# Optimization experiments

Hardware: AMD Instinct MI355X
Metric: run time of the kernel (lower is better)

The kernel has to match this reference:

```python
import jax, jax.numpy as jnp
import numpy as np

DT_RANK = 64
D_STATE = 16


def setup_inputs() -> dict:
    key = jax.random.key(0)
    ks = jax.random.split(key, 6)
    B, L, Di = 2, 2048, 2048
    x = jax.random.normal(ks[0], (B, L, Di), dtype=jnp.float32)
    W_xproj = jax.random.normal(ks[1], (DT_RANK + 2 * D_STATE, Di), dtype=jnp.float32) * (Di ** -0.5)
    W_dt = jax.random.uniform(ks[2], (Di, DT_RANK), dtype=jnp.float32, minval=-(DT_RANK ** -0.5), maxval=DT_RANK ** -0.5)
    dt = jnp.exp(jax.random.uniform(ks[3], (Di,), dtype=jnp.float32) * (np.log(0.1) - np.log(0.001)) + np.log(0.001))
    b_dt = dt + jnp.log(-jnp.expm1(-dt))
    A_log = jnp.log(jnp.broadcast_to(jnp.arange(1, D_STATE + 1, dtype=jnp.float32), (Di, D_STATE)))
    D_param = jnp.ones((Di,), dtype=jnp.float32)
    return {"x": x, "W_xproj": W_xproj, "W_dt": W_dt, "b_dt": b_dt, "A_log": A_log, "D_param": D_param}


def _selective_scan(u, delta, A, Bm, Cm):
    # u, delta: (b, l, d); A: (d, n); Bm, Cm: (b, l, n)
    deltaA = jnp.exp(delta[..., None] * A[None, None])          # (b, l, d, n)
    deltaB_u = delta[..., None] * Bm[:, :, None, :] * u[..., None]  # (b, l, d, n)

    def step(h, inp):
        dA, dBu, c = inp                      # dA,dBu: (b,d,n); c: (b,n)
        h = dA * h + dBu
        y = jnp.einsum('bdn,bn->bd', h, c)
        return h, y

    b, l, d = u.shape
    h0 = jnp.zeros((b, d, A.shape[1]), dtype=u.dtype)
    xs = (jnp.moveaxis(deltaA, 1, 0), jnp.moveaxis(deltaB_u, 1, 0), jnp.moveaxis(Cm, 1, 0))
    _, ys = jax.lax.scan(step, h0, xs)        # ys: (l, b, d)
    return jnp.moveaxis(ys, 0, 1)


def reference(x, W_xproj, W_dt, b_dt, A_log, D_param):
    x_dbl = jnp.einsum('bld,ed->ble', x, W_xproj)  # (b, l, dt_rank + 2*n)
    dlt = x_dbl[..., :DT_RANK]
    Bm = x_dbl[..., DT_RANK:DT_RANK + D_STATE]
    Cm = x_dbl[..., DT_RANK + D_STATE:]
    delta = jax.nn.softplus(jnp.einsum('blr,dr->bld', dlt, W_dt) + b_dt)
    A = -jnp.exp(A_log.astype(jnp.float32))
    y = _selective_scan(x, delta, A, Bm, Cm)
    return y + x * D_param[None, None, :]
```

## Files before the change

### kernel.cpp

```cpp
#include <hip/hip_runtime.h>

#define BATCH 2
#define L_SEQ 2048
#define DI 2048
#define NROW (BATCH * L_SEQ)
#define E_DIM 96
#define RNK 64
#define NST 16
#define NCH 64
#define CL 32
#define SPLITK 16
#define KSL (DI / SPLITK)

#define WS_XDBL 0
#define WS_PART 393216
#define WS_HLOC 393216
#define WS_DSUM (393216 + 4194304)

__device__ __forceinline__ float softplusf(float z) {
    return fmaxf(z, 0.f) + __logf(1.f + __expf(-fabsf(z)));
}

__global__ __launch_bounds__(256) void gemm_xproj_part(const float* __restrict__ x,
                                                       const float* __restrict__ Wx,
                                                       float* __restrict__ part) {
    __shared__ float xs[32][68];
    __shared__ float wsh[32][100];
    const int tid = threadIdx.x;
    const int r0 = blockIdx.x * 64;
    const int kbase0 = blockIdx.y * KSL;
    const int rg = tid >> 4;
    const int cg = tid & 15;

    float acc[4][6];
#pragma unroll
    for (int i = 0; i < 4; i++)
#pragma unroll
        for (int j = 0; j < 6; j++) acc[i][j] = 0.f;

    for (int kt = 0; kt < KSL / 32; kt++) {
        const int kb = kbase0 + kt * 32;
#pragma unroll
        for (int rep = 0; rep < 2; rep++) {
            int i = rep * 256 + tid;
            int row = i >> 3;
            int kq = i & 7;
            float4 v = *(const float4*)&x[(long)(r0 + row) * DI + kb + kq * 4];
            xs[kq * 4 + 0][row] = v.x;
            xs[kq * 4 + 1][row] = v.y;
            xs[kq * 4 + 2][row] = v.z;
            xs[kq * 4 + 3][row] = v.w;
        }
#pragma unroll
        for (int rep = 0; rep < 3; rep++) {
            int i = rep * 256 + tid;
            int e = i >> 3;
            int kq = i & 7;
            float4 v = *(const float4*)&Wx[(long)e * DI + kb + kq * 4];
            wsh[kq * 4 + 0][e] = v.x;
            wsh[kq * 4 + 1][e] = v.y;
            wsh[kq * 4 + 2][e] = v.z;
            wsh[kq * 4 + 3][e] = v.w;
        }
        __syncthreads();
#pragma unroll 8
        for (int k = 0; k < 32; k++) {
            float xr[4], wr[6];
#pragma unroll
            for (int i = 0; i < 4; i++) xr[i] = xs[k][rg * 4 + i];
#pragma unroll
            for (int j = 0; j < 6; j++) wr[j] = wsh[k][cg * 6 + j];
#pragma unroll
            for (int i = 0; i < 4; i++)
#pragma unroll
                for (int j = 0; j < 6; j++) acc[i][j] = fmaf(xr[i], wr[j], acc[i][j]);
        }
        __syncthreads();
    }
    const long sbase = (long)blockIdx.y * NROW * E_DIM;
#pragma unroll
    for (int i = 0; i < 4; i++) {
        long rowb = sbase + (long)(r0 + rg * 4 + i) * E_DIM + cg * 6;
#pragma unroll
        for (int j = 0; j < 6; j++) part[rowb + j] = acc[i][j];
    }
}

__global__ __launch_bounds__(256) void xproj_reduce(const float* __restrict__ part,
                                                    float* __restrict__ xdbl) {
    const int i4 = blockIdx.x * 256 + threadIdx.x;
    const float4* p4 = (const float4*)part;
    float4 s = p4[i4];
#pragma unroll
    for (int sp = 1; sp < SPLITK; sp++) {
        float4 v = p4[(long)sp * (NROW * E_DIM / 4) + i4];
        s.x += v.x; s.y += v.y; s.z += v.z; s.w += v.w;
    }
    ((float4*)xdbl)[i4] = s;
}

__global__ __launch_bounds__(256) void scan_carry_fused(const float* __restrict__ x,
                                                        const float* __restrict__ xdbl,
                                                        const float* __restrict__ Wdt,
                                                        const float* __restrict__ bdt,
                                                        const float* __restrict__ A_log,
                                                        float* __restrict__ delta_out,
                                                        float* __restrict__ hloc,
                                                        float* __restrict__ dsumb) {
    const int tid = threadIdx.x;
    const int d = blockIdx.x * 256 + tid;
    const int c = blockIdx.y;
    const int b = blockIdx.z;
    const int row0 = b * L_SEQ + c * CL;

    float wdtr[64];
#pragma unroll
    for (int q = 0; q < 16; q++) {
        float4 v = *(const float4*)&Wdt[(long)d * RNK + q * 4];
        wdtr[q * 4 + 0] = v.x; wdtr[q * 4 + 1] = v.y;
        wdtr[q * 4 + 2] = v.z; wdtr[q * 4 + 3] = v.w;
    }
    const float bd = bdt[d];

    float A[16];
#pragma unroll
    for (int q = 0; q < 4; q++) {
        float4 v = *(const float4*)&A_log[(long)d * NST + q * 4];
        A[q * 4 + 0] = -__expf(v.x);
        A[q * 4 + 1] = -__expf(v.y);
        A[q * 4 + 2] = -__expf(v.z);
        A[q * 4 + 3] = -__expf(v.w);
    }
    float h[16];
#pragma unroll
    for (int n = 0; n < 16; n++) h[n] = 0.f;
    float dsum = 0.f;

    long idx = (long)row0 * DI + d;
    float xn = x[idx];
    const float* __restrict__ rp = xdbl + (long)row0 * E_DIM;
    for (int ll = 0; ll < CL; ll++) {
        float xc = xn;
        if (ll + 1 < CL) xn = x[idx + DI];
        float dv0 = 0.f, dv1 = 0.f, dv2 = 0.f, dv3 = 0.f;
#pragma unroll
        for (int q = 0; q < 16; q++) {
            dv0 = fmaf(rp[q * 4 + 0], wdtr[q * 4 + 0], dv0);
            dv1 = fmaf(rp[q * 4 + 1], wdtr[q * 4 + 1], dv1);
            dv2 = fmaf(rp[q * 4 + 2], wdtr[q * 4 + 2], dv2);
            dv3 = fmaf(rp[q * 4 + 3], wdtr[q * 4 + 3], dv3);
        }
        float dc = softplusf(((dv0 + dv1) + (dv2 + dv3)) + bd);
        delta_out[idx] = dc;
        float du = dc * xc;
#pragma unroll
        for (int n = 0; n < 16; n++)
            h[n] = fmaf(__expf(dc * A[n]), h[n], du * rp[64 + n]);
        dsum += dc;
        idx += DI;
        rp += E_DIM;
    }

    const long cb = ((long)(b * NCH + c) * DI + d);
#pragma unroll
    for (int q = 0; q < 4; q++)
        *(float4*)&hloc[cb * 16 + q * 4] =
            make_float4(h[q * 4], h[q * 4 + 1], h[q * 4 + 2], h[q * 4 + 3]);
    dsumb[cb] = dsum;
}

__global__ __launch_bounds__(256) void scan_prefix(const float* __restrict__ A_log,
                                                   float* __restrict__ hloc,
                                                   const float* __restrict__ dsumb) {
    const int g = blockIdx.x * 256 + threadIdx.x;
    const int n = g & 15;
    const int d = (g >> 4) & (DI - 1);
    const int b = g >> 15;
    const float An = -__expf(A_log[(long)d * NST + n]);
    float hc = 0.f;
    for (int c = 0; c < NCH; c++) {
        const long cb = ((long)(b * NCH + c) * DI + d);
        float hl = hloc[cb * 16 + n];
        float dsv = dsumb[cb];
        hloc[cb * 16 + n] = hc;
        hc = fmaf(__expf(An * dsv), hc, hl);
    }
}

__global__ __launch_bounds__(256) void scan_out(const float* __restrict__ x,
                                                const float* __restrict__ xdbl,
                                                const float* __restrict__ A_log,
                                                const float* __restrict__ Dp,
                                                const float* __restrict__ hloc,
                                                float* __restrict__ out) {
    const int tid = threadIdx.x;
    const int d = blockIdx.x * 256 + tid;
    const int c = blockIdx.y;
    const int b = blockIdx.z;
    const int row0 = b * L_SEQ + c * CL;

    float A[16];
#pragma unroll
    for (int q = 0; q < 4; q++) {
        float4 v = *(const float4*)&A_log[(long)d * NST + q * 4];
        A[q * 4 + 0] = -__expf(v.x);
        A[q * 4 + 1] = -__expf(v.y);
        A[q * 4 + 2] = -__expf(v.z);
        A[q * 4 + 3] = -__expf(v.w);
    }
    float h[16];
    const long cb = ((long)(b * NCH + c) * DI + d);
#pragma unroll
    for (int q = 0; q < 4; q++) {
        float4 v = *(const float4*)&hloc[cb * 16 + q * 4];
        h[q * 4 + 0] = v.x; h[q * 4 + 1] = v.y; h[q * 4 + 2] = v.z; h[q * 4 + 3] = v.w;
    }
    const float Dd = Dp[d];

    long idx = (long)row0 * DI + d;
    float dn = out[idx], xn = x[idx];
    const float* __restrict__ rp = xdbl + (long)row0 * E_DIM;
    for (int ll = 0; ll < CL; ll++) {
        float dc = dn, xc = xn;
        long nidx = (ll + 1 < CL) ? idx + DI : idx;
        dn = out[nidx];
        xn = x[nidx];
        float du = dc * xc;
        float y = 0.f;
#pragma unroll
        for (int n = 0; n < 16; n++) {
            h[n] = fmaf(__expf(dc * A[n]), h[n], du * rp[64 + n]);
            y = fmaf(h[n], rp[80 + n], y);
        }
        out[idx] = fmaf(xc, Dd, y);
        idx += DI;
        rp += E_DIM;
    }
}

extern "C" void kernel_launch(void* const* d_in, const int* in_sizes, int n_in,
                              void* d_out, int out_size, void* d_ws, size_t ws_size,
                              hipStream_t stream) {
    const float* x    = (const float*)d_in[0];
    const float* Wx   = (const float*)d_in[1];
    const float* Wdt  = (const float*)d_in[2];
    const float* bdt  = (const float*)d_in[3];
    const float* Alog = (const float*)d_in[4];
    const float* Dp   = (const float*)d_in[5];
    float* out = (float*)d_out;
    float* ws = (float*)d_ws;
    float* xdbl  = ws + WS_XDBL;
    float* partb = ws + WS_PART;
    float* hloc  = ws + WS_HLOC;
    float* dsumb = ws + WS_DSUM;

    gemm_xproj_part<<<dim3(NROW / 64, SPLITK), 256, 0, stream>>>(x, Wx, partb);
    xproj_reduce<<<dim3(NROW * E_DIM / 4 / 256), 256, 0, stream>>>(partb, xdbl);
    scan_carry_fused<<<dim3(DI / 256, NCH, BATCH), 256, 0, stream>>>(x, xdbl, Wdt, bdt,
                                                                     Alog, out, hloc, dsumb);
    scan_prefix<<<dim3(BATCH * DI * NST / 256), 256, 0, stream>>>(Alog, hloc, dsumb);
    scan_out<<<dim3(DI / 256, NCH, BATCH), 256, 0, stream>>>(x, xdbl, Alog, Dp, hloc, out);
}
```

Baseline: 216.4 us.

## Split delta projection into tiled shared-memory GEMM and stage B/C in LDS

Moves the dt-rank projection and softplus out of the scan carry kernel into a dedicated register- and LDS-tiled GEMM that writes delta to the output buffer. The scan kernels read delta from memory and load each chunk's B and C rows into shared memory once per block, rather than every thread reading them from global memory. This removes the 64-float Wdt register array and the per-thread 64-FMA dot product from the latency-bound scan. The cost is an extra kernel launch plus a full write and re-read of delta through global memory.

New measurement: 201.5 us. 6.9% less time.

```diff
diff --git a/kernel.cpp b/kernel.cpp
--- a/kernel.cpp
+++ b/kernel.cpp
@@ -99,28 +99,95 @@
     ((float4*)xdbl)[i4] = s;
 }
 
-__global__ __launch_bounds__(256) void scan_carry_fused(const float* __restrict__ x,
-                                                        const float* __restrict__ xdbl,
-                                                        const float* __restrict__ Wdt,
-                                                        const float* __restrict__ bdt,
-                                                        const float* __restrict__ A_log,
-                                                        float* __restrict__ delta_out,
-                                                        float* __restrict__ hloc,
-                                                        float* __restrict__ dsumb) {
+__global__ __launch_bounds__(256) void gemm_dt(const float* __restrict__ xdbl,
+                                               const float* __restrict__ Wdt,
+                                               const float* __restrict__ b_dt,
+                                               float* __restrict__ delta) {
+    __shared__ float dl[32][68];
+    __shared__ float wt[32][132];
+    const int tid = threadIdx.x;
+    const int row0 = blockIdx.x * 64;
+    const int d0 = blockIdx.y * 128;
+    const int rg = tid >> 5;
+    const int cg = tid & 31;
+
+    float acc[8][4];
+#pragma unroll
+    for (int i = 0; i < 8; i++)
+#pragma unroll
+        for (int j = 0; j < 4; j++) acc[i][j] = 0.f;
+
+    for (int kt = 0; kt < 2; kt++) {
+        const int kb = kt * 32;
+#pragma unroll
+        for (int rep = 0; rep < 2; rep++) {
+            int i = rep * 256 + tid;
+            int row = i >> 3;
+            int kq = i & 7;
+            float4 v = *(const float4*)&xdbl[(long)(row0 + row) * E_DIM + kb + kq * 4];
+            dl[kq * 4 + 0][row] = v.x;
+            dl[kq * 4 + 1][row] = v.y;
+            dl[kq * 4 + 2][row] = v.z;
+            dl[kq * 4 + 3][row] = v.w;
+        }
+#pragma unroll
+        for (int rep = 0; rep < 4; rep++) {
+            int i = rep * 256 + tid;
+            int col = i >> 3;
+            int kq = i & 7;
+            float4 v = *(const float4*)&Wdt[(long)(d0 + col) * RNK + kb + kq * 4];
+            wt[kq * 4 + 0][col] = v.x;
+            wt[kq * 4 + 1][col] = v.y;
+            wt[kq * 4 + 2][col] = v.z;
+            wt[kq * 4 + 3][col] = v.w;
+        }
+        __syncthreads();
+#pragma unroll 8
+        for (int k = 0; k < 32; k++) {
+            float xr[8], wr[4];
+#pragma unroll
+            for (int i = 0; i < 8; i++) xr[i] = dl[k][rg * 8 + i];
+#pragma unroll
+            for (int j = 0; j < 4; j++) wr[j] = wt[k][cg * 4 + j];
+#pragma unroll
+            for (int i = 0; i < 8; i++)
+#pragma unroll
+                for (int j = 0; j < 4; j++) acc[i][j] = fmaf(xr[i], wr[j], acc[i][j]);
+        }
+        __syncthreads();
+    }
+
+    float4 bb = *(const float4*)&b_dt[d0 + cg * 4];
+#pragma unroll
+    for (int i = 0; i < 8; i++) {
+        int row = row0 + rg * 8 + i;
+        float4 o;
+        o.x = softplusf(acc[i][0] + bb.x);
+        o.y = softplusf(acc[i][1] + bb.y);
+        o.z = softplusf(acc[i][2] + bb.z);
+        o.w = softplusf(acc[i][3] + bb.w);
+        *(float4*)&delta[(long)row * DI + d0 + cg * 4] = o;
+    }
+}
+
+__global__ __launch_bounds__(256) void scan_carry(const float* __restrict__ x,
+                                                  const float* __restrict__ delta,
+                                                  const float* __restrict__ xdbl,
+                                                  const float* __restrict__ A_log,
+                                                  float* __restrict__ hloc,
+                                                  float* __restrict__ dsumb) {
+    __shared__ float bs[CL * NST];
     const int tid = threadIdx.x;
     const int d = blockIdx.x * 256 + tid;
     const int c = blockIdx.y;
     const int b = blockIdx.z;
     const int row0 = b * L_SEQ + c * CL;
 
-    float wdtr[64];
-#pragma unroll
-    for (int q = 0; q < 16; q++) {
-        float4 v = *(const float4*)&Wdt[(long)d * RNK + q * 4];
-        wdtr[q * 4 + 0] = v.x; wdtr[q * 4 + 1] = v.y;
-        wdtr[q * 4 + 2] = v.z; wdtr[q * 4 + 3] = v.w;
-    }
-    const float bd = bdt[d];
+    for (int i = tid; i < CL * NST / 4; i += 256) {
+        int row = i >> 2, q = i & 3;
+        ((float4*)bs)[i] = *(const float4*)&xdbl[(long)(row0 + row) * E_DIM + 64 + q * 4];
+    }
+    __syncthreads();
 
     float A[16];
 #pragma unroll
@@ -137,28 +204,22 @@
     float dsum = 0.f;
 
     long idx = (long)row0 * DI + d;
-    float xn = x[idx];
-    const float* __restrict__ rp = xdbl + (long)row0 * E_DIM;
+    float dn = delta[idx], xn = x[idx];
     for (int ll = 0; ll < CL; ll++) {
-        float xc = xn;
-        if (ll + 1 < CL) xn = x[idx + DI];
-        float dv0 = 0.f, dv1 = 0.f, dv2 = 0.f, dv3 = 0.f;
-#pragma unroll
-        for (int q = 0; q < 16; q++) {
-            dv0 = fmaf(rp[q * 4 + 0], wdtr[q * 4 + 0], dv0);
-            dv1 = fmaf(rp[q * 4 + 1], wdtr[q * 4 + 1], dv1);
-            dv2 = fmaf(rp[q * 4 + 2], wdtr[q * 4 + 2], dv2);
-            dv3 = fmaf(rp[q * 4 + 3], wdtr[q * 4 + 3], dv3);
-        }
-        float dc = softplusf(((dv0 + dv1) + (dv2 + dv3)) + bd);
-        delta_out[idx] = dc;
+        float dc = dn, xc = xn;
+        if (ll + 1 < CL) { dn = delta[idx + DI]; xn = x[idx + DI]; }
         float du = dc * xc;
+        float bl[16];
+#pragma unroll
+        for (int q = 0; q < 4; q++) {
+            float4 v = *(const float4*)&bs[ll * NST + q * 4];
+            bl[q * 4 + 0] = v.x; bl[q * 4 + 1] = v.y; bl[q * 4 + 2] = v.z; bl[q * 4 + 3] = v.w;
+        }
 #pragma unroll
         for (int n = 0; n < 16; n++)
-            h[n] = fmaf(__expf(dc * A[n]), h[n], du * rp[64 + n]);
+            h[n] = fmaf(__expf(dc * A[n]), h[n], du * bl[n]);
         dsum += dc;
         idx += DI;
-        rp += E_DIM;
     }
 
     const long cb = ((long)(b * NCH + c) * DI + d);
@@ -193,11 +254,20 @@
                                                 const float* __restrict__ Dp,
                                                 const float* __restrict__ hloc,
                                                 float* __restrict__ out) {
+    __shared__ float bs[CL * NST];
+    __shared__ float cs[CL * NST];
     const int tid = threadIdx.x;
     const int d = blockIdx.x * 256 + tid;
     const int c = blockIdx.y;
     const int b = blockIdx.z;
     const int row0 = b * L_SEQ + c * CL;
+
+    for (int i = tid; i < CL * NST / 4; i += 256) {
+        int row = i >> 2, q = i & 3;
+        ((float4*)bs)[i] = *(const float4*)&xdbl[(long)(row0 + row) * E_DIM + 64 + q * 4];
+        ((float4*)cs)[i] = *(const float4*)&xdbl[(long)(row0 + row) * E_DIM + 80 + q * 4];
+    }
+    __syncthreads();
 
     float A[16];
 #pragma unroll
@@ -219,22 +289,30 @@
 
     long idx = (long)row0 * DI + d;
     float dn = out[idx], xn = x[idx];
-    const float* __restrict__ rp = xdbl + (long)row0 * E_DIM;
     for (int ll = 0; ll < CL; ll++) {
         float dc = dn, xc = xn;
-        long nidx = (ll + 1 < CL) ? idx + DI : idx;
-        dn = out[nidx];
-        xn = x[nidx];
+        if (ll + 1 < CL) { dn = out[idx + DI]; xn = x[idx + DI]; }
         float du = dc * xc;
         float y = 0.f;
 #pragma unroll
-        for (int n = 0; n < 16; n++) {
-            h[n] = fmaf(__expf(dc * A[n]), h[n], du * rp[64 + n]);
-            y = fmaf(h[n], rp[80 + n], y);
+        for (int q = 0; q < 4; q++) {
+            float4 v = *(const float4*)&bs[ll * NST + q * 4];
+            float4 w = *(const float4*)&cs[ll * NST + q * 4];
+            float e0 = __expf(dc * A[q * 4 + 0]);
+            float e1 = __expf(dc * A[q * 4 + 1]);
+            float e2 = __expf(dc * A[q * 4 + 2]);
+            float e3 = __expf(dc * A[q * 4 + 3]);
+            h[q * 4 + 0] = fmaf(e0, h[q * 4 + 0], du * v.x);
+            h[q * 4 + 1] = fmaf(e1, h[q * 4 + 1], du * v.y);
+            h[q * 4 + 2] = fmaf(e2, h[q * 4 + 2], du * v.z);
+            h[q * 4 + 3] = fmaf(e3, h[q * 4 + 3], du * v.w);
+            y = fmaf(h[q * 4 + 0], w.x, y);
+            y = fmaf(h[q * 4 + 1], w.y, y);
+            y = fmaf(h[q * 4 + 2], w.z, y);
+            y = fmaf(h[q * 4 + 3], w.w, y);
         }
         out[idx] = fmaf(xc, Dd, y);
         idx += DI;
-        rp += E_DIM;
     }
 }
 
@@ -256,8 +334,8 @@
 
     gemm_xproj_part<<<dim3(NROW / 64, SPLITK), 256, 0, stream>>>(x, Wx, partb);
     xproj_reduce<<<dim3(NROW * E_DIM / 4 / 256), 256, 0, stream>>>(partb, xdbl);
-    scan_carry_fused<<<dim3(DI / 256, NCH, BATCH), 256, 0, stream>>>(x, xdbl, Wdt, bdt,
-                                                                     Alog, out, hloc, dsumb);
+    gemm_dt<<<dim3(NROW / 64, DI / 128), 256, 0, stream>>>(xdbl, Wdt, bdt, out);
+    scan_carry<<<dim3(DI / 256, NCH, BATCH), 256, 0, stream>>>(x, out, xdbl, Alog, hloc, dsumb);
     scan_prefix<<<dim3(BATCH * DI * NST / 256), 256, 0, stream>>>(Alog, hloc, dsumb);
     scan_out<<<dim3(DI / 256, NCH, BATCH), 256, 0, stream>>>(x, xdbl, Alog, Dp, hloc, out);
 }
```

## Recompute delta in both scan passes instead of storing it to global

Applied to the files above, without the earlier changes.

Stops writing delta to global memory in the carry pass and reading it back in the output pass. Both scan kernels now recompute delta from the dt-rank slice of xdbl, which is staged in shared memory, using a chunk-wide dot-product precompute. B and C are also staged in LDS and read as float4. This saves 32MB of global write plus read traffic, in exchange for a duplicated 64-wide dot product per element, more registers (ddot[32]) and a launch_bounds occupancy hint.

Result: slower. 234.3 us (+8.3%).

```diff
diff --git a/kernel.cpp b/kernel.cpp
--- a/kernel.cpp
+++ b/kernel.cpp
@@ -99,26 +99,59 @@
     ((float4*)xdbl)[i4] = s;
 }
 
-__global__ __launch_bounds__(256) void scan_carry_fused(const float* __restrict__ x,
+__global__ __launch_bounds__(256, 4) void scan_carry_dt(const float* __restrict__ x,
                                                         const float* __restrict__ xdbl,
                                                         const float* __restrict__ Wdt,
                                                         const float* __restrict__ bdt,
                                                         const float* __restrict__ A_log,
-                                                        float* __restrict__ delta_out,
                                                         float* __restrict__ hloc,
                                                         float* __restrict__ dsumb) {
+    __shared__ float dlt_s[CL][RNK];
+    __shared__ float bs[CL * NST];
     const int tid = threadIdx.x;
     const int d = blockIdx.x * 256 + tid;
     const int c = blockIdx.y;
     const int b = blockIdx.z;
     const int row0 = b * L_SEQ + c * CL;
 
-    float wdtr[64];
-#pragma unroll
-    for (int q = 0; q < 16; q++) {
-        float4 v = *(const float4*)&Wdt[(long)d * RNK + q * 4];
-        wdtr[q * 4 + 0] = v.x; wdtr[q * 4 + 1] = v.y;
-        wdtr[q * 4 + 2] = v.z; wdtr[q * 4 + 3] = v.w;
+    for (int i = tid; i < CL * 16; i += 256) {
+        int row = i >> 4, q = i & 15;
+        *(float4*)&dlt_s[row][q * 4] =
+            *(const float4*)&xdbl[(long)(row0 + row) * E_DIM + q * 4];
+    }
+    for (int i = tid; i < CL * 4; i += 256) {
+        int row = i >> 2, q = i & 3;
+        ((float4*)bs)[i] = *(const float4*)&xdbl[(long)(row0 + row) * E_DIM + 64 + q * 4];
+    }
+    __syncthreads();
+
+    float ddot[CL];
+#pragma unroll
+    for (int l = 0; l < CL; l++) ddot[l] = 0.f;
+#pragma unroll
+    for (int kq = 0; kq < 4; kq++) {
+        const float* wp = &Wdt[(long)d * RNK + kq * 16];
+        float4 w0 = *(const float4*)&wp[0];
+        float4 w1 = *(const float4*)&wp[4];
+        float4 w2 = *(const float4*)&wp[8];
+        float4 w3 = *(const float4*)&wp[12];
+#pragma unroll
+        for (int l = 0; l < CL; l++) {
+            float4 s0 = *(const float4*)&dlt_s[l][kq * 16 + 0];
+            float4 s1 = *(const float4*)&dlt_s[l][kq * 16 + 4];
+            float4 s2 = *(const float4*)&dlt_s[l][kq * 16 + 8];
+            float4 s3 = *(const float4*)&dlt_s[l][kq * 16 + 12];
+            float t = ddot[l];
+            t = fmaf(s0.x, w0.x, t); t = fmaf(s0.y, w0.y, t);
+            t = fmaf(s0.z, w0.z, t); t = fmaf(s0.w, w0.w, t);
+            t = fmaf(s1.x, w1.x, t); t = fmaf(s1.y, w1.y, t);
+            t = fmaf(s1.z, w1.z, t); t = fmaf(s1.w, w1.w, t);
+            t = fmaf(s2.x, w2.x, t); t = fmaf(s2.y, w2.y, t);
+            t = fmaf(s2.z, w2.z, t); t = fmaf(s2.w, w2.w, t);
+            t = fmaf(s3.x, w3.x, t); t = fmaf(s3.y, w3.y, t);
+            t = fmaf(s3.z, w3.z, t); t = fmaf(s3.w, w3.w, t);
+            ddot[l] = t;
+        }
     }
     const float bd = bdt[d];
 
@@ -138,27 +171,22 @@
 
     long idx = (long)row0 * DI + d;
     float xn = x[idx];
-    const float* __restrict__ rp = xdbl + (long)row0 * E_DIM;
+#pragma unroll 4
     for (int ll = 0; ll < CL; ll++) {
         float xc = xn;
         if (ll + 1 < CL) xn = x[idx + DI];
-        float dv0 = 0.f, dv1 = 0.f, dv2 = 0.f, dv3 = 0.f;
-#pragma unroll
-        for (int q = 0; q < 16; q++) {
-            dv0 = fmaf(rp[q * 4 + 0], wdtr[q * 4 + 0], dv0);
-            dv1 = fmaf(rp[q * 4 + 1], wdtr[q * 4 + 1], dv1);
-            dv2 = fmaf(rp[q * 4 + 2], wdtr[q * 4 + 2], dv2);
-            dv3 = fmaf(rp[q * 4 + 3], wdtr[q * 4 + 3], dv3);
-        }
-        float dc = softplusf(((dv0 + dv1) + (dv2 + dv3)) + bd);
-        delta_out[idx] = dc;
+        float dc = softplusf(ddot[ll] + bd);
         float du = dc * xc;
 #pragma unroll
-        for (int n = 0; n < 16; n++)
-            h[n] = fmaf(__expf(dc * A[n]), h[n], du * rp[64 + n]);
+        for (int q = 0; q < 4; q++) {
+            float4 v = *(const float4*)&bs[ll * NST + q * 4];
+            h[q * 4 + 0] = fmaf(__expf(dc * A[q * 4 + 0]), h[q * 4 + 0], du * v.x);
+            h[q * 4 + 1] = fmaf(__expf(dc * A[q * 4 + 1]), h[q * 4 + 1], du * v.y);
+            h[q * 4 + 2] = fmaf(__expf(dc * A[q * 4 + 2]), h[q * 4 + 2], du * v.z);
+            h[q * 4 + 3] = fmaf(__expf(dc * A[q * 4 + 3]), h[q * 4 + 3], du * v.w);
+        }
         dsum += dc;
         idx += DI;
-        rp += E_DIM;
     }
 
     const long cb = ((long)(b * NCH + c) * DI + d);
@@ -187,17 +215,64 @@
     }
 }
 
-__global__ __launch_bounds__(256) void scan_out(const float* __restrict__ x,
-                                                const float* __restrict__ xdbl,
-                                                const float* __restrict__ A_log,
-                                                const float* __restrict__ Dp,
-                                                const float* __restrict__ hloc,
-                                                float* __restrict__ out) {
+__global__ __launch_bounds__(256, 4) void scan_out_dt(const float* __restrict__ x,
+                                                      const float* __restrict__ xdbl,
+                                                      const float* __restrict__ Wdt,
+                                                      const float* __restrict__ bdt,
+                                                      const float* __restrict__ A_log,
+                                                      const float* __restrict__ Dp,
+                                                      const float* __restrict__ hloc,
+                                                      float* __restrict__ out) {
+    __shared__ float dlt_s[CL][RNK];
+    __shared__ float bs[CL * NST];
+    __shared__ float cs[CL * NST];
     const int tid = threadIdx.x;
     const int d = blockIdx.x * 256 + tid;
     const int c = blockIdx.y;
     const int b = blockIdx.z;
     const int row0 = b * L_SEQ + c * CL;
+
+    for (int i = tid; i < CL * 16; i += 256) {
+        int row = i >> 4, q = i & 15;
+        *(float4*)&dlt_s[row][q * 4] =
+            *(const float4*)&xdbl[(long)(row0 + row) * E_DIM + q * 4];
+    }
+    for (int i = tid; i < CL * 4; i += 256) {
+        int row = i >> 2, q = i & 3;
+        ((float4*)bs)[i] = *(const float4*)&xdbl[(long)(row0 + row) * E_DIM + 64 + q * 4];
+        ((float4*)cs)[i] = *(const float4*)&xdbl[(long)(row0 + row) * E_DIM + 80 + q * 4];
+    }
+    __syncthreads();
+
+    float ddot[CL];
+#pragma unroll
+    for (int l = 0; l < CL; l++) ddot[l] = 0.f;
+#pragma unroll
+    for (int kq = 0; kq < 4; kq++) {
+        const float* wp = &Wdt[(long)d * RNK + kq * 16];
+        float4 w0 = *(const float4*)&wp[0];
+        float4 w1 = *(const float4*)&wp[4];
+        float4 w2 = *(const float4*)&wp[8];
+        float4 w3 = *(const float4*)&wp[12];
+#pragma unroll
+        for (int l = 0; l < CL; l++) {
+            float4 s0 = *(const float4*)&dlt_s[l][kq * 16 + 0];
+            float4 s1 = *(const float4*)&dlt_s[l][kq * 16 + 4];
+            float4 s2 = *(const float4*)&dlt_s[l][kq * 16 + 8];
+            float4 s3 = *(const float4*)&dlt_s[l][kq * 16 + 12];
+            float t = ddot[l];
+            t = fmaf(s0.x, w0.x, t); t = fmaf(s0.y, w0.y, t);
+            t = fmaf(s0.z, w0.z, t); t = fmaf(s0.w, w0.w, t);
+            t = fmaf(s1.x, w1.x, t); t = fmaf(s1.y, w1.y, t);
+            t = fmaf(s1.z, w1.z, t); t = fmaf(s1.w, w1.w, t);
+            t = fmaf(s2.x, w2.x, t); t = fmaf(s2.y, w2.y, t);
+            t = fmaf(s2.z, w2.z, t); t = fmaf(s2.w, w2.w, t);
+            t = fmaf(s3.x, w3.x, t); t = fmaf(s3.y, w3.y, t);
+            t = fmaf(s3.z, w3.z, t); t = fmaf(s3.w, w3.w, t);
+            ddot[l] = t;
+        }
+    }
+    const float bd = bdt[d];
 
     float A[16];
 #pragma unroll
@@ -218,23 +293,29 @@
     const float Dd = Dp[d];
 
     long idx = (long)row0 * DI + d;
-    float dn = out[idx], xn = x[idx];
-    const float* __restrict__ rp = xdbl + (long)row0 * E_DIM;
+    float xn = x[idx];
+#pragma unroll 4
     for (int ll = 0; ll < CL; ll++) {
-        float dc = dn, xc = xn;
-        long nidx = (ll + 1 < CL) ? idx + DI : idx;
-        dn = out[nidx];
-        xn = x[nidx];
+        float xc = xn;
+        if (ll + 1 < CL) xn = x[idx + DI];
+        float dc = softplusf(ddot[ll] + bd);
         float du = dc * xc;
         float y = 0.f;
 #pragma unroll
-        for (int n = 0; n < 16; n++) {
-            h[n] = fmaf(__expf(dc * A[n]), h[n], du * rp[64 + n]);
-            y = fmaf(h[n], rp[80 + n], y);
+        for (int q = 0; q < 4; q++) {
+            float4 v = *(const float4*)&bs[ll * NST + q * 4];
+            float4 w = *(const float4*)&cs[ll * NST + q * 4];
+            h[q * 4 + 0] = fmaf(__expf(dc * A[q * 4 + 0]), h[q * 4 + 0], du * v.x);
+            h[q * 4 + 1] = fmaf(__expf(dc * A[q * 4 + 1]), h[q * 4 + 1], du * v.y);
+            h[q * 4 + 2] = fmaf(__expf(dc * A[q * 4 + 2]), h[q * 4 + 2], du * v.z);
+            h[q * 4 + 3] = fmaf(__expf(dc * A[q * 4 + 3]), h[q * 4 + 3], du * v.w);
+            y = fmaf(h[q * 4 + 0], w.x, y);
+            y = fmaf(h[q * 4 + 1], w.y, y);
+            y = fmaf(h[q * 4 + 2], w.z, y);
+            y = fmaf(h[q * 4 + 3], w.w, y);
         }
         out[idx] = fmaf(xc, Dd, y);
         idx += DI;
-        rp += E_DIM;
     }
 }
 
@@ -256,8 +337,9 @@
 
     gemm_xproj_part<<<dim3(NROW / 64, SPLITK), 256, 0, stream>>>(x, Wx, partb);
     xproj_reduce<<<dim3(NROW * E_DIM / 4 / 256), 256, 0, stream>>>(partb, xdbl);
-    scan_carry_fused<<<dim3(DI / 256, NCH, BATCH), 256, 0, stream>>>(x, xdbl, Wdt, bdt,
-                                                                     Alog, out, hloc, dsumb);
+    scan_carry_dt<<<dim3(DI / 256, NCH, BATCH), 256, 0, stream>>>(x, xdbl, Wdt, bdt,
+                                                                  Alog, hloc, dsumb);
     scan_prefix<<<dim3(BATCH * DI * NST / 256), 256, 0, stream>>>(Alog, hloc, dsumb);
-    scan_out<<<dim3(DI / 256, NCH, BATCH), 256, 0, stream>>>(x, xdbl, Alog, Dp, hloc, out);
-}
+    scan_out_dt<<<dim3(DI / 256, NCH, BATCH), 256, 0, stream>>>(x, xdbl, Wdt, bdt,
+                                                                Alog, Dp, hloc, out);
+}
```
